# Optimization experiments

Measured on AMD Instinct MI355X. Metric: run time of the kernel, lower is better.

## Reference

```python
import jax, jax.numpy as jnp
import numpy as np

RADIUS = 0.1
WEIGHT = 0.2
MATMUL_NORM = False


def setup_inputs() -> dict:
    key = jax.random.key(0)
    k1, k2, k3, k4, k5 = jax.random.split(key, 5)
    S, B, Ck, Cv, H, W = 8, 2, 64, 64, 64, 64
    return {
        "memory_keys": jax.random.normal(k1, (S, B, Ck, H, W), jnp.float32),
        "memory_values": jax.random.normal(k2, (S, B, Cv, H, W), jnp.float32),
        "query_query": jax.random.normal(k3, (B, Ck, H, W), jnp.float32),
        "disparity": jax.random.normal(k4, (B, 1, H, W), jnp.float32),
        "sequence_index": jax.random.randint(k5, (B, S, 2), 0, 10, jnp.int32),
    }


def reference(memory_keys, memory_values, query_query, disparity, sequence_index):
    S, B, Ck, H, W = memory_keys.shape
    Cv = memory_values.shape[2]
    HW, SHW = H * W, S * H * W

    # keys: [B, Ck, S*H*W]; queries: [B, H*W, Ck]
    keys = jnp.transpose(memory_keys, (1, 2, 0, 3, 4)).reshape(B, Ck, SHW)
    q = jnp.transpose(query_query.reshape(B, Ck, HW), (0, 2, 1))

    # disparity-based additive mask, vectorized over frames
    weight = WEIGHT / S / H / W
    idx = sequence_index.astype(jnp.float32)
    dist = jnp.sqrt((idx[:, :, 1] - 5.0) ** 2 + (idx[:, :, 0] - 5.0) ** 2)  # [B, S]
    total_disp = dist[:, :, None, None] * disparity  # [B, S, H, W] (disparity [B,1,H,W])
    mask = jnp.where(jnp.abs(total_disp) > RADIUS, weight, 0.0).reshape(B, 1, SHW)

    attn = jnp.einsum("bnc,bcm->bnm", q, keys)  # [B, HW, SHW]
    if MATMUL_NORM:
        attn = attn * (Ck ** -0.5)
    attn = jax.nn.softmax(attn, axis=-1) + mask

    vals = jnp.transpose(memory_values, (1, 0, 3, 4, 2)).reshape(B, SHW, Cv)
    out = jnp.einsum("bnm,bmv->bnv", attn, vals)  # [B, HW, Cv]
    return jnp.transpose(out, (0, 2, 1)).reshape(B, Cv, H, W)
```

## Files before the change

### kernel.cpp

```cpp
#include <hip/hip_runtime.h>
#include <hip/hip_bf16.h>
#include <stdint.h>

#define NS   8
#define NB   2
#define CK   64
#define CV   64
#define HWN  4096
#define SHW  32768
#define RADIUS_ 0.1f
#define MASK_W  6.103515625e-6f

#define TM    32
#define NW    8
#define QS_STR 68
#define P_STR  40
#define SBIAS 24.0f
#define KS    4

#define KT_ELEMS (NS * NB * CK * HWN)
#define KT_BYTES ((size_t)KT_ELEMS * 2)
#define VB_BYTES ((size_t)KT_ELEMS * 2)
#define MASK_OFF (KT_BYTES + VB_BYTES)
#define WS_NEED  (MASK_OFF + (size_t)NB * CV * 4)
#define ONUM_OFF (MASK_OFF + 4096)
#define ONUM_BYTES ((size_t)KS * NB * HWN * CV * 4)
#define ODEN_OFF (ONUM_OFF + ONUM_BYTES)
#define ODEN_BYTES ((size_t)KS * NB * HWN * 4)
#define WS2      (ODEN_OFF + ODEN_BYTES)

typedef __bf16    bf16x8 __attribute__((ext_vector_type(8)));
typedef _Float16  f16x8  __attribute__((ext_vector_type(8)));
typedef float     f32x4  __attribute__((ext_vector_type(4)));
typedef unsigned short u16x8 __attribute__((ext_vector_type(8)));

__device__ __forceinline__ unsigned short f2bfu(float x) {
  __hip_bfloat16 h = __float2bfloat16(x);
  return __builtin_bit_cast(unsigned short, h);
}
__device__ __forceinline__ bf16x8 ld_bf8_lds(const unsigned short* p) {
  u16x8 u = *(const u16x8*)p;
  return __builtin_bit_cast(bf16x8, u);
}
__device__ __forceinline__ void load_lds16(const void* g, void* l) {
  __builtin_amdgcn_global_load_lds(
      (const __attribute__((address_space(1))) unsigned int*)g,
      (__attribute__((address_space(3))) unsigned int*)l, 16, 0, 0);
}

#define PK_STR 72
__global__ __launch_bounds__(512) void prep_all(
    const float* __restrict__ keys, const float* __restrict__ vals,
    const float* __restrict__ disp, const int* __restrict__ seq,
    _Float16* __restrict__ kT, unsigned short* __restrict__ vbf,
    float* __restrict__ maskadd)
{
  const int t = threadIdx.x;
  const int blk = blockIdx.x;
  if (blk < 256) {
    __shared__ _Float16 lds[256 * PK_STR];
    const int chunk = blk & 15;
    const int s     = (blk >> 4) & 7;
    const int b     = blk >> 7;
    const int hw0   = chunk * 256;
    const int c_st  = t >> 3;
    const int msub  = (t & 7) * 8;

    const float* krow = keys + ((size_t)((s * NB + b) * CK + c_st)) * HWN + hw0;
    #pragma unroll
    for (int r = 0; r < 4; ++r) {
      const int m0 = msub + r * 64;
      f32x4 k0 = *(const f32x4*)(krow + m0);
      f32x4 k1 = *(const f32x4*)(krow + m0 + 4);
      #pragma unroll
      for (int j = 0; j < 4; ++j) {
        lds[(m0 + j)     * PK_STR + c_st] = (_Float16)k0[j];
        lds[(m0 + 4 + j) * PK_STR + c_st] = (_Float16)k1[j];
      }
    }
    __syncthreads();

    _Float16* kout = kT + ((size_t)(b * SHW + s * HWN + hw0)) * CK;
    const int mm = t >> 3, c0 = (t & 7) * 8;
    #pragma unroll
    for (int r2 = 0; r2 < 4; ++r2) {
      const int m = mm + r2 * 64;
      u16x8 v = *(const u16x8*)&lds[m * PK_STR + c0];
      *(u16x8*)(kout + (size_t)m * CK + c0) = v;
    }
  } else {
    const int r = blk - 256;
    const int s = r >> 7;
    const int b = (r >> 6) & 1;
    const int c = r & 63;
    float j0 = (float)seq[(b * NS + s) * 2 + 0];
    float j1 = (float)seq[(b * NS + s) * 2 + 1];
    const float dist = sqrtf((j1 - 5.f) * (j1 - 5.f) + (j0 - 5.f) * (j0 - 5.f));

    const size_t i = (size_t)r * HWN + t * 8;
    const int hw = t * 8;
    f32x4 a  = *(const f32x4*)(vals + i);
    f32x4 bb = *(const f32x4*)(vals + i + 4);
    f32x4 d0 = *(const f32x4*)(disp + (size_t)b * HWN + hw);
    f32x4 d1 = *(const f32x4*)(disp + (size_t)b * HWN + hw + 4);
    u16x8 o;
    float acc = 0.f;
    #pragma unroll
    for (int j = 0; j < 4; ++j) {
      o[j]     = f2bfu(a[j]);
      o[4 + j] = f2bfu(bb[j]);
      if (fabsf(dist * d0[j]) > RADIUS_) acc += a[j];
      if (fabsf(dist * d1[j]) > RADIUS_) acc += bb[j];
    }
    *(u16x8*)(vbf + i) = o;

    #pragma unroll
    for (int m = 32; m >= 1; m >>= 1) acc += __shfl_xor(acc, m);
    __shared__ float red[8];
    if ((t & 63) == 0) red[t >> 6] = acc;
    __syncthreads();
    if (t == 0) {
      float s8 = 0.f;
      #pragma unroll
      for (int j = 0; j < 8; ++j) s8 += red[j];
      atomicAdd(&maskadd[b * CV + c], MASK_W * s8);
    }
  }
}

struct __align__(16) Smem6 {
  union {
    struct {
      _Float16       kbuf[2][128 * 64];
      unsigned short vbuf[2][64 * 128];
      unsigned short p[NW][16 * P_STR];
    } main;
    struct {
      float obuf[4][32][64];
      float dbuf[4][32];
    } epi;
    float qs[64 * QS_STR];
  };
};

__global__ __launch_bounds__(512, 4) void attn_v6(
    const _Float16* __restrict__ kT,
    const unsigned short* __restrict__ vbf,
    const float* __restrict__ query,
    float* __restrict__ onum,
    float* __restrict__ odenom)
{
  __shared__ Smem6 sm;
  const int t    = threadIdx.x;
  const int w    = t >> 6;
  const int lane = t & 63;
  const int quad = lane >> 4;
  const int l15  = lane & 15;
  const int kq   = w & 3;
  const int rg   = w >> 2;
  const int bidx = blockIdx.x;
  const int xcd  = bidx & 7;
  const int b    = xcd & 1;
  const int ks   = xcd >> 1;
  const int tile = bidx >> 3;
  const int n0   = tile * 64;

  {
    const int qc   = t >> 3;
    const int noff = (t & 7) * 8;
    const int slot = qc ^ ((t & 7) << 2);
    const float* qp = query + (size_t)(b * CK + qc) * HWN + n0 + noff;
    f32x4 q0 = *(const f32x4*)(qp);
    f32x4 q1 = *(const f32x4*)(qp + 4);
    #pragma unroll
    for (int j = 0; j < 4; ++j) {
      sm.qs[(noff + j)     * QS_STR + slot] = q0[j];
      sm.qs[(noff + 4 + j) * QS_STR + slot] = q1[j];
    }
  }
  __syncthreads();
  f16x8 qf[2][2];
  #pragma unroll
  for (int f = 0; f < 2; ++f) {
    const int n  = rg * 32 + f * 16 + l15;
    const int sw = ((n >> 3) & 7) << 2;
    const float* base = &sm.qs[n * QS_STR];
    #pragma unroll
    for (int h = 0; h < 2; ++h) {
      const int c0 = (h * 32 + quad * 8) ^ sw;
      f32x4 a  = *(const f32x4*)(base + c0);
      f32x4 bb = *(const f32x4*)(base + (c0 ^ 4));
      f16x8 q;
      #pragma unroll
      for (int j = 0; j < 4; ++j) { q[j] = (_Float16)a[j]; q[4 + j] = (_Float16)bb[j]; }
      qf[f][h] = q;
    }
  }
  __syncthreads();

  f32x4 Of[2][4];
  f32x4 Ol[2];
  #pragma unroll
  for (int f = 0; f < 2; ++f) {
    #pragma unroll
    for (int cf = 0; cf < 4; ++cf) Of[f][cf] = (f32x4){0.f, 0.f, 0.f, 0.f};
    Ol[f] = (f32x4){0.f, 0.f, 0.f, 0.f};
  }
  bf16x8 vones;
  #pragma unroll
  for (int i = 0; i < 8; ++i)
    vones[i] = __builtin_bit_cast(__bf16, (unsigned short)0x3F80);

  uint32_t ksrc_off[2];
  int      kldsoff[2];
  uint32_t vsrc_off[2];
  int      vldsoff[2];
  #pragma unroll
  for (int j = 0; j < 2; ++j) {
    const int inst = w * 2 + j;
    const int kl   = inst * 8 + (lane >> 3);
    const int cqs  = lane & 7;
    ksrc_off[j] = (uint32_t)(kl * 128 + ((cqs ^ (kl & 7)) * 16));
    kldsoff[j]  = inst * 1024;
    const int cv  = inst * 4 + (lane >> 4);
    const int chs = (lane & 15) ^ (cv & 7);
    vsrc_off[j] = (uint32_t)(cv * HWN + chs * 8);
    vldsoff[j]  = inst * 1024;
  }
  const char* kgbase = (const char*)(kT + (size_t)b * SHW * CK);
  const int   kbase0 = ks * (SHW / KS);

  {
    const char* kg = kgbase + (size_t)kbase0 * 128;
    load_lds16(kg + ksrc_off[0], (char*)sm.main.kbuf[0] + kldsoff[0]);
    load_lds16(kg + ksrc_off[1], (char*)sm.main.kbuf[0] + kldsoff[1]);
    const int sfrm0 = kbase0 >> 12;
    const unsigned short* vg =
        vbf + (size_t)((sfrm0 * NB + b) * CV) * HWN + (kbase0 & 4095);
    load_lds16(vg + vsrc_off[0], (char*)sm.main.vbuf[0] + vldsoff[0]);
    load_lds16(vg + vsrc_off[1], (char*)sm.main.vbuf[0] + vldsoff[1]);
  }

  for (int it = 0; it < 64; ++it) {
    const int cur  = it & 1;
    const int key0 = kbase0 + it * 128;

    __syncthreads();

    if (it < 63) {
      const int keyn = key0 + 128;
      const char* kg = kgbase + (size_t)keyn * 128;
      load_lds16(kg + ksrc_off[0], (char*)sm.main.kbuf[cur ^ 1] + kldsoff[0]);
      load_lds16(kg + ksrc_off[1], (char*)sm.main.kbuf[cur ^ 1] + kldsoff[1]);
      const int sfrmn = keyn >> 12;
      const unsigned short* vg =
          vbf + (size_t)((sfrmn * NB + b) * CV) * HWN + (keyn & 4095);
      load_lds16(vg + vsrc_off[0], (char*)sm.main.vbuf[cur ^ 1] + vldsoff[0]);
      load_lds16(vg + vsrc_off[1], (char*)sm.main.vbuf[cur ^ 1] + vldsoff[1]);
    }

    f16x8 kf[2][2];
    #pragma unroll
    for (int g = 0; g < 2; ++g) {
      const int kl  = kq * 32 + g * 16 + l15;
      const int swz = kl & 7;
      const _Float16* kb = &sm.main.kbuf[cur][kl * 64];
      #pragma unroll
      for (int h = 0; h < 2; ++h) {
        const int slot = (h * 4 + quad) ^ swz;
        kf[g][h] = *(const f16x8*)(kb + slot * 8);
      }
    }

    bf16x8 vf[4];
    #pragma unroll
    for (int cf = 0; cf < 4; ++cf) {
      const int cv = cf * 16 + l15;
      const int c  = (kq * 4 + quad) ^ (cv & 7);
      vf[cf] = ld_bf8_lds(&sm.main.vbuf[cur][cv * 128 + c * 8]);
    }

    f32x4 sf[2][2];
    #pragma unroll
    for (int g = 0; g < 2; ++g)
      #pragma unroll
      for (int f = 0; f < 2; ++f) {
        f32x4 acc = (f32x4){0.f, 0.f, 0.f, 0.f};
        acc = __builtin_amdgcn_mfma_f32_16x16x32_f16(kf[g][0], qf[f][0], acc, 0, 0, 0);
        acc = __builtin_amdgcn_mfma_f32_16x16x32_f16(kf[g][1], qf[f][1], acc, 0, 0, 0);
        sf[g][f] = acc;
      }

    #pragma unroll
    for (int f = 0; f < 2; ++f) {
      #pragma unroll
      for (int g = 0; g < 2; ++g) {
        float e0 = __expf(sf[g][f][0] - SBIAS);
        float e1 = __expf(sf[g][f][1] - SBIAS);
        float e2 = __expf(sf[g][f][2] - SBIAS);
        float e3 = __expf(sf[g][f][3] - SBIAS);
        uint2 pk;
        pk.x = (__builtin_bit_cast(unsigned, e0) >> 16) |
               (__builtin_bit_cast(unsigned, e1) & 0xFFFF0000u);
        pk.y = (__builtin_bit_cast(unsigned, e2) >> 16) |
               (__builtin_bit_cast(unsigned, e3) & 0xFFFF0000u);
        *(uint2*)((char*)&sm.main.p[w][0] + l15 * 80 + g * 32 + quad * 8) = pk;
      }
      asm volatile("s_waitcnt lgkmcnt(0)" ::: "memory");
      bf16x8 pf = ld_bf8_lds(&sm.main.p[w][l15 * P_STR + quad * 8]);

      #pragma unroll
      for (int cf = 0; cf < 4; ++cf)
        Of[f][cf] = __builtin_amdgcn_mfma_f32_16x16x32_bf16(pf, vf[cf], Of[f][cf], 0, 0, 0);
      Ol[f] = __builtin_amdgcn_mfma_f32_16x16x32_bf16(pf, vones, Ol[f], 0, 0, 0);
    }
  }

  __syncthreads();

  #pragma unroll
  for (int phase = 0; phase < 2; ++phase) {
    if (rg == phase) {
      #pragma unroll
      for (int f = 0; f < 2; ++f)
        #pragma unroll
        for (int r = 0; r < 4; ++r) {
          const int row = f * 16 + quad * 4 + r;
          if (l15 == 0) sm.epi.dbuf[kq][row] = Ol[f][r];
          #pragma unroll
          for (int cf = 0; cf < 4; ++cf)
            sm.epi.obuf[kq][row][cf * 16 + l15] = Of[f][cf][r];
        }
    }
    __syncthreads();
    {
      const int row = t >> 4;
      const int v4  = (t & 15) * 4;
      f32x4 acc = *(const f32x4*)&sm.epi.obuf[0][row][v4];
      #pragma unroll
      for (int q = 1; q < 4; ++q)
        acc += *(const f32x4*)&sm.epi.obuf[q][row][v4];
      *(f32x4*)&onum[((size_t)(ks * NB + b) * HWN + n0 + phase * 32 + row) * CV + v4] = acc;
      if (t < 32) {
        float d = sm.epi.dbuf[0][t] + sm.epi.dbuf[1][t] +
                  sm.epi.dbuf[2][t] + sm.epi.dbuf[3][t];
        odenom[(size_t)(ks * NB + b) * HWN + n0 + phase * 32 + t] = d;
      }
    }
    __syncthreads();
  }
}

__global__ __launch_bounds__(256) void finalize_k(
    const float* __restrict__ onum, const float* __restrict__ odenom,
    const float* __restrict__ maskadd, float* __restrict__ out)
{
  __shared__ float tile[64][68];
  __shared__ float dinv[64];
  __shared__ float ml[64];
  const int t   = threadIdx.x;
  const int b   = blockIdx.x >> 6;
  const int hw0 = (blockIdx.x & 63) * 64;

  #pragma unroll
  for (int pass = 0; pass < 4; ++pass) {
    const int row = pass * 16 + (t >> 4);
    const int v4  = (t & 15) * 4;
    f32x4 acc = (f32x4){0.f, 0.f, 0.f, 0.f};
    #pragma unroll
    for (int ks = 0; ks < KS; ++ks)
      acc += *(const f32x4*)&onum[((size_t)(ks * NB + b) * HWN + hw0 + row) * CV + v4];
    *(f32x4*)&tile[row][v4] = acc;
  }
  if (t < 64) {
    float d = 0.f;
    #pragma unroll
    for (int ks = 0; ks < KS; ++ks)
      d += odenom[(size_t)(ks * NB + b) * HWN + hw0 + t];
    dinv[t] = 1.f / fmaxf(d, 1e-30f);
  }
  if (t >= 64 && t < 128) ml[t - 64] = maskadd[b * CV + (t - 64)];
  __syncthreads();

  #pragma unroll
  for (int pass = 0; pass < 4; ++pass) {
    const int v   = pass * 16 + (t >> 4);
    const int hw4 = (t & 15) * 4;
    f32x4 o;
    #pragma unroll
    for (int j = 0; j < 4; ++j)
      o[j] = tile[hw4 + j][v] * dinv[hw4 + j] + ml[v];
    *(f32x4*)&out[((size_t)(b * CV + v)) * HWN + hw0 + hw4] = o;
  }
}

struct __align__(16) SmemF {
  union {
    float qs[TM * QS_STR];
    unsigned short p[NW][2][16 * P_STR];
    struct {
      float obuf[NW][TM][CV];
      float lbuf[NW][TM];
    } epi;
  };
};

__global__ __launch_bounds__(512) void attn_fast(
    const _Float16* __restrict__ kT, const unsigned short* __restrict__ vbf,
    const float* __restrict__ query, const float* __restrict__ maskadd,
    float* __restrict__ out)
{
  __shared__ SmemF sm;
  const int t    = threadIdx.x;
  const int w    = t >> 6;
  const int lane = t & 63;
  const int quad = lane >> 4;
  const int l15  = lane & 15;
  const int bidx = blockIdx.x;
  const int b    = bidx & 1;
  const int n0   = ((bidx >> 1) & 127) * TM;

  if (t < 256) {
    const int qc   = t >> 2;
    const int noff = (t & 3) * 8;
    const int slot = qc ^ ((t & 3) << 2);
    const float* qp = query + (size_t)(b * CK + qc) * HWN + n0 + noff;
    f32x4 q0 = *(const f32x4*)(qp);
    f32x4 q1 = *(const f32x4*)(qp + 4);
    #pragma unroll
    for (int j = 0; j < 4; ++j) {
      sm.qs[(noff + j)     * QS_STR + slot] = q0[j];
      sm.qs[(noff + 4 + j) * QS_STR + slot] = q1[j];
    }
  }
  __syncthreads();
  f16x8 qf[2][2];
  #pragma unroll
  for (int f = 0; f < 2; ++f) {
    const int n  = f * 16 + l15;
    const int sw = ((n >> 3) & 7) << 2;
    const float* base = &sm.qs[n * QS_STR];
    #pragma unroll
    for (int h = 0; h < 2; ++h) {
      const int c0 = (h * 32 + quad * 8) ^ sw;
      f32x4 a  = *(const f32x4*)(base + c0);
      f32x4 bb = *(const f32x4*)(base + (c0 ^ 4));
      f16x8 q;
      #pragma unroll
      for (int j = 0; j < 4; ++j) { q[j] = (_Float16)a[j]; q[4 + j] = (_Float16)bb[j]; }
      qf[f][h] = q;
    }
  }
  __syncthreads();

  f32x4 Of[2][4];
  f32x4 Ol[2];
  #pragma unroll
  for (int f = 0; f < 2; ++f) {
    #pragma unroll
    for (int cf = 0; cf < 4; ++cf) Of[f][cf] = (f32x4){0.f, 0.f, 0.f, 0.f};
    Ol[f] = (f32x4){0.f, 0.f, 0.f, 0.f};
  }
  bf16x8 vones;
  #pragma unroll
  for (int i = 0; i < 8; ++i)
    vones[i] = __builtin_bit_cast(__bf16, (unsigned short)0x3F80);

  const _Float16* kbase = kT + (size_t)b * SHW * CK;

  for (int it = 0; it < SHW / 256; ++it) {
    const int key0 = it * 256 + w * 32;
    f16x8 kf[2][2];
    #pragma unroll
    for (int g = 0; g < 2; ++g)
      #pragma unroll
      for (int h = 0; h < 2; ++h)
        kf[g][h] = *(const f16x8*)(kbase +
            (size_t)(key0 + g * 16 + l15) * CK + h * 32 + quad * 8);

    const int s   = it >> 4;
    const int hwv = (it & 15) * 256 + w * 32 + quad * 8;
    bf16x8 vf[4];
    #pragma unroll
    for (int cf = 0; cf < 4; ++cf)
      vf[cf] = ld_bf8_lds(vbf +
          ((size_t)((s * NB + b) * CV + cf * 16 + l15)) * HWN + hwv);

    f32x4 sfv[2][2];
    #pragma unroll
    for (int f = 0; f < 2; ++f)
      #pragma unroll
      for (int g = 0; g < 2; ++g) {
        f32x4 acc = (f32x4){0.f, 0.f, 0.f, 0.f};
        acc = __builtin_amdgcn_mfma_f32_16x16x32_f16(qf[f][0], kf[g][0], acc, 0, 0, 0);
        acc = __builtin_amdgcn_mfma_f32_16x16x32_f16(qf[f][1], kf[g][1], acc, 0, 0, 0);
        sfv[f][g] = acc;
      }

    #pragma unroll
    for (int f = 0; f < 2; ++f)
      #pragma unroll
      for (int g = 0; g < 2; ++g)
        #pragma unroll
        for (int r = 0; r < 4; ++r)
          sfv[f][g][r] = __expf(sfv[f][g][r] - SBIAS);

    #pragma unroll
    for (int f = 0; f < 2; ++f)
      #pragma unroll
      for (int g = 0; g < 2; ++g)
        #pragma unroll
        for (int r = 0; r < 4; ++r)
          sm.p[w][f][(quad * 4 + r) * P_STR + g * 16 + l15] = f2bfu(sfv[f][g][r]);
    asm volatile("s_waitcnt lgkmcnt(0)" ::: "memory");
    bf16x8 pf[2];
    #pragma unroll
    for (int f = 0; f < 2; ++f)
      pf[f] = ld_bf8_lds(&sm.p[w][f][l15 * P_STR + quad * 8]);

    #pragma unroll
    for (int f = 0; f < 2; ++f) {
      #pragma unroll
      for (int cf = 0; cf < 4; ++cf)
        Of[f][cf] = __builtin_amdgcn_mfma_f32_16x16x32_bf16(pf[f], vf[cf], Of[f][cf], 0, 0, 0);
      Ol[f] = __builtin_amdgcn_mfma_f32_16x16x32_bf16(pf[f], vones, Ol[f], 0, 0, 0);
    }
  }

  __syncthreads();
  #pragma unroll
  for (int f = 0; f < 2; ++f)
    #pragma unroll
    for (int r = 0; r < 4; ++r) {
      const int row = f * 16 + quad * 4 + r;
      if (l15 == 0) sm.epi.lbuf[w][row] = Ol[f][r];
      #pragma unroll
      for (int cf = 0; cf < 4; ++cf)
        sm.epi.obuf[w][row][cf * 16 + l15] = Of[f][cf][r];
    }
  __syncthreads();
  {
    const int n   = t & 31;
    const int vhi = t >> 5;
    float denom = 0.f;
    #pragma unroll
    for (int ww = 0; ww < NW; ++ww) denom += sm.epi.lbuf[ww][n];
    const float inv = 1.f / fmaxf(denom, 1e-30f);
    #pragma unroll
    for (int g = 0; g < 4; ++g) {
      const int v = vhi + 16 * g;
      float num = 0.f;
      #pragma unroll
      for (int ww = 0; ww < NW; ++ww) num += sm.epi.obuf[ww][n][v];
      out[((size_t)(b * CV + v)) * HWN + n0 + n] = num * inv + maskadd[b * CV + v];
    }
  }
}

extern "C" void kernel_launch(void* const* d_in, const int* in_sizes, int n_in,
                              void* d_out, int out_size, void* d_ws, size_t ws_size,
                              hipStream_t stream) {
  const float* keys  = (const float*)d_in[0];
  const float* vals  = (const float*)d_in[1];
  const float* query = (const float*)d_in[2];
  const float* disp  = (const float*)d_in[3];
  const int*   seq   = (const int*)d_in[4];
  float*       out   = (float*)d_out;

  _Float16*       kT   = (_Float16*)d_ws;
  unsigned short* vbf  = (unsigned short*)((char*)d_ws + KT_BYTES);
  float*          mask = (float*)((char*)d_ws + MASK_OFF);

  hipMemsetAsync(mask, 0, (size_t)NB * CV * 4, stream);
  prep_all<<<256 + NB * NS * CV, 512, 0, stream>>>(keys, vals, disp, seq, kT, vbf, mask);

  if (ws_size >= WS2) {
    float* onum   = (float*)((char*)d_ws + ONUM_OFF);
    float* odenom = (float*)((char*)d_ws + ODEN_OFF);
    attn_v6<<<NB * 64 * KS, 512, 0, stream>>>(kT, vbf, query, onum, odenom);
    finalize_k<<<NB * (HWN / 64), 256, 0, stream>>>(onum, odenom, mask, out);
  } else {
    attn_fast<<<NB * (HWN / TM), 512, 0, stream>>>(kT, vbf, query, mask, out);
  }
}
```

Baseline: 183.3 us.

## Keep softmax probabilities in registers, fold bias and log2e into MFMA

Removes the per-wave LDS round trip used to reshape the exp'd scores into the PV MFMA A-operand. The V fragment loads are rearranged so the k-ordering matches the register layout the QK MFMA output already has. It also pre-scales the queries by log2(e) and seeds the accumulator with the negative bias, so a raw exp2 replaces expf-with-subtract. Bf16 packing now uses v_perm. The risks are an extra fp16 rounding on the scaled queries and a permuted, less vectorized V load pattern.

```diff
diff --git a/kernel.cpp b/kernel.cpp
--- a/kernel.cpp
+++ b/kernel.cpp
@@ -16,6 +16,8 @@
 #define QS_STR 68
 #define P_STR  40
 #define SBIAS 24.0f
+#define LOG2E 1.4426950408889634f
+#define SBIAS2 34.624680981135326f
 #define KS    4
 
 #define KT_ELEMS (NS * NB * CK * HWN)
@@ -33,6 +35,8 @@
 typedef _Float16  f16x8  __attribute__((ext_vector_type(8)));
 typedef float     f32x4  __attribute__((ext_vector_type(4)));
 typedef unsigned short u16x8 __attribute__((ext_vector_type(8)));
+typedef uint32_t  u32x2 __attribute__((ext_vector_type(2)));
+typedef uint32_t  u32x4 __attribute__((ext_vector_type(4)));
 
 __device__ __forceinline__ unsigned short f2bfu(float x) {
   __hip_bfloat16 h = __float2bfloat16(x);
@@ -133,7 +137,6 @@
     struct {
       _Float16       kbuf[2][128 * 64];
       unsigned short vbuf[2][64 * 128];
-      unsigned short p[NW][16 * P_STR];
     } main;
     struct {
       float obuf[4][32][64];
@@ -192,7 +195,10 @@
       f32x4 bb = *(const f32x4*)(base + (c0 ^ 4));
       f16x8 q;
       #pragma unroll
-      for (int j = 0; j < 4; ++j) { q[j] = (_Float16)a[j]; q[4 + j] = (_Float16)bb[j]; }
+      for (int j = 0; j < 4; ++j) {
+        q[j]     = (_Float16)(a[j]  * LOG2E);
+        q[4 + j] = (_Float16)(bb[j] * LOG2E);
+      }
       qf[f][h] = q;
     }
   }
@@ -273,11 +279,18 @@
     }
 
     bf16x8 vf[4];
-    #pragma unroll
-    for (int cf = 0; cf < 4; ++cf) {
-      const int cv = cf * 16 + l15;
-      const int c  = (kq * 4 + quad) ^ (cv & 7);
-      vf[cf] = ld_bf8_lds(&sm.main.vbuf[cur][cv * 128 + c * 8]);
+    {
+      const int c0 = kq * 4 + (quad >> 1);
+      const int ho = (quad & 1) * 4;
+      #pragma unroll
+      for (int cf = 0; cf < 4; ++cf) {
+        const int cv  = cf * 16 + l15;
+        const int swz = cv & 7;
+        const unsigned short* row = &sm.main.vbuf[cur][cv * 128];
+        u32x2 lo = *(const u32x2*)(row + ((c0       ^ swz) * 8) + ho);
+        u32x2 hi = *(const u32x2*)(row + (((c0 + 2) ^ swz) * 8) + ho);
+        vf[cf] = __builtin_bit_cast(bf16x8, (u32x4){lo.x, lo.y, hi.x, hi.y});
+      }
     }
 
     f32x4 sf[2][2];
@@ -285,7 +298,7 @@
     for (int g = 0; g < 2; ++g)
       #pragma unroll
       for (int f = 0; f < 2; ++f) {
-        f32x4 acc = (f32x4){0.f, 0.f, 0.f, 0.f};
+        f32x4 acc = (f32x4){-SBIAS2, -SBIAS2, -SBIAS2, -SBIAS2};
         acc = __builtin_amdgcn_mfma_f32_16x16x32_f16(kf[g][0], qf[f][0], acc, 0, 0, 0);
         acc = __builtin_amdgcn_mfma_f32_16x16x32_f16(kf[g][1], qf[f][1], acc, 0, 0, 0);
         sf[g][f] = acc;
@@ -293,21 +306,22 @@
 
     #pragma unroll
     for (int f = 0; f < 2; ++f) {
+      uint32_t pk[2][2];
       #pragma unroll
       for (int g = 0; g < 2; ++g) {
-        float e0 = __expf(sf[g][f][0] - SBIAS);
-        float e1 = __expf(sf[g][f][1] - SBIAS);
-        float e2 = __expf(sf[g][f][2] - SBIAS);
-        float e3 = __expf(sf[g][f][3] - SBIAS);
-        uint2 pk;
-        pk.x = (__builtin_bit_cast(unsigned, e0) >> 16) |
-               (__builtin_bit_cast(unsigned, e1) & 0xFFFF0000u);
-        pk.y = (__builtin_bit_cast(unsigned, e2) >> 16) |
-               (__builtin_bit_cast(unsigned, e3) & 0xFFFF0000u);
-        *(uint2*)((char*)&sm.main.p[w][0] + l15 * 80 + g * 32 + quad * 8) = pk;
-      }
-      asm volatile("s_waitcnt lgkmcnt(0)" ::: "memory");
-      bf16x8 pf = ld_bf8_lds(&sm.main.p[w][l15 * P_STR + quad * 8]);
+        float e0 = __builtin_amdgcn_exp2f(sf[g][f][0]);
+        float e1 = __builtin_amdgcn_exp2f(sf[g][f][1]);
+        float e2 = __builtin_amdgcn_exp2f(sf[g][f][2]);
+        float e3 = __builtin_amdgcn_exp2f(sf[g][f][3]);
+        pk[g][0] = __builtin_amdgcn_perm(__builtin_bit_cast(uint32_t, e1),
+                                         __builtin_bit_cast(uint32_t, e0),
+                                         0x07060302u);
+        pk[g][1] = __builtin_amdgcn_perm(__builtin_bit_cast(uint32_t, e3),
+                                         __builtin_bit_cast(uint32_t, e2),
+                                         0x07060302u);
+      }
+      bf16x8 pf = __builtin_bit_cast(bf16x8,
+          (u32x4){pk[0][0], pk[0][1], pk[1][0], pk[1][1]});
 
       #pragma unroll
       for (int cf = 0; cf < 4; ++cf)
```

Result: faster. 172.3 us (-6.0%).
